# Kernel tuning notes

Measured on AMD Instinct MI355X. Metric: run time of the kernel, lower is better.

## Reference

```python
import jax, jax.numpy as jnp
import numpy as np
from jax import lax

B, D, H, W = 16, 256, 64, 64
P = 8  # patchsize
EPS = 1e-5


def setup_inputs() -> dict:
    key = jax.random.key(0)
    ks = jax.random.split(key, 8)
    s = 0.02
    return {
        "x": jax.random.normal(ks[0], (B, D, H, W), jnp.float32),
        "wq": jax.random.normal(ks[1], (D, D), jnp.float32) * s,
        "bq": jnp.zeros((D,), jnp.float32),
        "wk": jax.random.normal(ks[2], (D, D), jnp.float32) * s,
        "bk": jnp.zeros((D,), jnp.float32),
        "wv": jax.random.normal(ks[3], (D, D), jnp.float32) * s,
        "bv": jnp.zeros((D,), jnp.float32),
        "w_out": jax.random.normal(ks[4], (D, D, 3, 3), jnp.float32) * s,
        "b_out": jnp.zeros((D,), jnp.float32),
        "gamma": jnp.ones((D,), jnp.float32),
        "beta": jnp.zeros((D,), jnp.float32),
        "bn_mean": jnp.zeros((D,), jnp.float32),
        "bn_var": jnp.ones((D,), jnp.float32),
    }


def _conv1x1(x, w, b):
    # x: [b,c,h,w], w: [o,c] (1x1 conv) -> [b,o,h,w]
    return jnp.einsum('bchw,oc->bohw', x, w) + b[None, :, None, None]


def _to_patches(t, p):
    # [b,d,h,w] -> [b, p*p, d*hh*ww]  (matches view+permute(0,2,4,1,3,5)+view)
    b, d, h, w = t.shape
    hh, ww = h // p, w // p
    t = t.reshape(b, d, p, hh, p, ww).transpose(0, 2, 4, 1, 3, 5)
    return t.reshape(b, p * p, d * hh * ww)


def reference(x, wq, bq, wk, bk, wv, bv, w_out, b_out, gamma, beta, bn_mean, bn_var):
    b, d, h, w = x.shape
    p = P
    hh, ww = h // p, w // p

    q = _to_patches(_conv1x1(x, wq, bq), p)  # [b, p^2, d*hh*ww]
    k = _to_patches(_conv1x1(x, wk, bk), p)
    v = _to_patches(_conv1x1(x, wv, bv), p)

    scale = 1.0 / jnp.sqrt(jnp.asarray(q.shape[-1], q.dtype))
    scores = jnp.einsum('bqe,bke->bqk', q, k) * scale  # [b, p^2, p^2]
    attn = jax.nn.softmax(scores, axis=-1)
    out = jnp.einsum('bqk,bke->bqe', attn, v)  # [b, p^2, d*hh*ww]

    # [b,p,p,d,hh,ww] -> permute(0,3,1,4,2,5) -> [b,d,h,w]
    out = out.reshape(b, p, p, d, hh, ww).transpose(0, 3, 1, 4, 2, 5).reshape(b, d, h, w)

    # 3x3 conv, padding 1
    y = lax.conv_general_dilated(out, w_out, window_strides=(1, 1),
                                 padding=((1, 1), (1, 1)),
                                 dimension_numbers=('NCHW', 'OIHW', 'NCHW'))
    y = y + b_out[None, :, None, None]

    # BatchNorm2d (eval mode with running stats)
    inv = gamma / jnp.sqrt(bn_var + EPS)
    y = (y - bn_mean[None, :, None, None]) * inv[None, :, None, None] + beta[None, :, None, None]

    # LeakyReLU(0.2)
    return jnp.where(y >= 0, y, 0.2 * y)
```

## Files before the change

kernel.cpp:

```cpp
#include <hip/hip_runtime.h>
#include <hip/hip_bf16.h>

#define BB 16
#define SS 4096

typedef __attribute__((ext_vector_type(8))) short short8;
typedef __attribute__((ext_vector_type(4))) float float4v;

__global__ __launch_bounds__(256) void wprep_all(
    const float* __restrict__ wo, const float* __restrict__ wq,
    const float* __restrict__ wk, const float* __restrict__ wv,
    __hip_bfloat16* __restrict__ blob, __hip_bfloat16* __restrict__ blob_a) {
  const int bid = blockIdx.x;
  const int tid = threadIdx.x;
  if (bid < 288) {
    int chunk = bid * 256 + tid;
    int l = chunk & 63;
    int ob = (chunk >> 6) & 15;
    int cb = (chunk >> 10) & 7;
    int tap = chunk >> 13;
    int o = ob * 16 + (l & 15);
    int c0 = cb * 32 + (l >> 4) * 8;
    union { uint4 u; __hip_bfloat16 h[8]; } t;
#pragma unroll
    for (int j = 0; j < 8; ++j)
      t.h[j] = __float2bfloat16(wo[((size_t)(o * 256 + c0 + j)) * 9 + tap]);
    *reinterpret_cast<uint4*>(blob + (size_t)chunk * 8) = t.u;
  } else {
    int chunk = (bid - 288) * 256 + tid;
    int lane = chunk & 63;
    int ob = (chunk >> 6) & 15;
    int cb = (chunk >> 10) & 7;
    int which = chunk >> 13;
    const float* W = (which == 0) ? wq : (which == 1) ? wk : wv;
    int o = ob * 16 + (lane & 15);
    int c0 = cb * 32 + (lane >> 4) * 8;
    const float* p = W + o * 256 + c0;
    union { uint4 u; __hip_bfloat16 h[8]; } t;
#pragma unroll
    for (int j = 0; j < 8; ++j) t.h[j] = __float2bfloat16(p[j]);
    *reinterpret_cast<uint4*>(blob_a + (size_t)chunk * 8) = t.u;
  }
}

__global__ __launch_bounds__(256, 4) void qkv_mfma(
    const float* __restrict__ x, const __hip_bfloat16* __restrict__ blob,
    const float* __restrict__ bq, const float* __restrict__ bk,
    const float* __restrict__ bv,
    __hip_bfloat16* __restrict__ qb, __hip_bfloat16* __restrict__ kb,
    __hip_bfloat16* __restrict__ vb) {
  __shared__ short ls[2][64 * 40];
  const int which = blockIdx.z;
  const int b = blockIdx.y;
  const int s0 = blockIdx.x * 64;
  const float* bias = (which == 0) ? bq : (which == 1) ? bk : bv;
  __hip_bfloat16* outb = (which == 0) ? qb : kb;
  const int tid = threadIdx.x;
  const int wave = tid >> 6, lane = tid & 63;
  const int q = lane >> 4, m = lane & 15;
  const int sl = tid & 63;
  const int cg = tid >> 6;
  float4v acc[4][4] = {};

  const float* xbase = x + ((size_t)(b * 256 + cg * 8)) * SS + s0 + sl;
  float xr[8];
#pragma unroll
  for (int i = 0; i < 8; ++i) xr[i] = xbase[(size_t)i * SS];
  {
    union { uint4 u; __hip_bfloat16 h[8]; } t;
#pragma unroll
    for (int i = 0; i < 8; ++i) t.h[i] = __float2bfloat16(xr[i]);
    *reinterpret_cast<uint4*>(&ls[0][sl * 40 + cg * 8]) = t.u;
  }
  __syncthreads();

  for (int cb = 0; cb < 8; ++cb) {
    const short* cur = ls[cb & 1];
    short* nxt = ls[(cb + 1) & 1];
    if (cb < 7) {
#pragma unroll
      for (int i = 0; i < 8; ++i)
        xr[i] = xbase[(size_t)(cb + 1) * 32 * SS + (size_t)i * SS];
    }
    short8 af[4];
#pragma unroll
    for (int of = 0; of < 4; ++of)
      af[of] = *reinterpret_cast<const short8*>(
          blob +
          ((size_t)(((which * 8 + cb) * 16 + wave * 4 + of) * 64 + lane)) * 8);
    short8 xf[4];
#pragma unroll
    for (int sf = 0; sf < 4; ++sf)
      xf[sf] =
          *reinterpret_cast<const short8*>(&cur[(sf * 16 + m) * 40 + q * 8]);
#pragma unroll
    for (int of = 0; of < 4; ++of)
#pragma unroll
      for (int sf = 0; sf < 4; ++sf)
        acc[of][sf] = __builtin_amdgcn_mfma_f32_16x16x32_bf16(
            af[of], xf[sf], acc[of][sf], 0, 0, 0);
    if (cb < 7) {
      union { uint4 u; __hip_bfloat16 h[8]; } t;
#pragma unroll
      for (int i = 0; i < 8; ++i) t.h[i] = __float2bfloat16(xr[i]);
      *reinterpret_cast<uint4*>(&nxt[sl * 40 + cg * 8]) = t.u;
    }
    __syncthreads();
  }
  if (which == 2) {
    const int h = s0 >> 6;
#pragma unroll
    for (int of = 0; of < 4; ++of) {
      int o_base = wave * 64 + of * 16 + q * 4;
#pragma unroll
      for (int sf = 0; sf < 4; ++sf) {
        int w = sf * 16 + m;
        union { uint2 u; __hip_bfloat16 hh[4]; } t;
#pragma unroll
        for (int r = 0; r < 4; ++r)
          t.hh[r] = __float2bfloat16(acc[of][sf][r] + bias[o_base + r]);
        *reinterpret_cast<uint2*>(
            vb + ((size_t)((b * 64 + h) * 64 + w)) * 256 + o_base) = t.u;
      }
    }
  } else {
#pragma unroll
    for (int of = 0; of < 4; ++of) {
      int o_base = wave * 64 + of * 16 + q * 4;
#pragma unroll
      for (int r = 0; r < 4; ++r) {
        int o = o_base + r;
        float bi = bias[o];
        __hip_bfloat16* op = outb + ((size_t)(b * 256 + o)) * SS + s0 + m;
#pragma unroll
        for (int sf = 0; sf < 4; ++sf)
          op[sf * 16] = __float2bfloat16(acc[of][sf][r] + bi);
      }
    }
  }
}

__global__ __launch_bounds__(256) void scores_mfma(
    const __hip_bfloat16* __restrict__ qb, const __hip_bfloat16* __restrict__ kb,
    float* __restrict__ part) {
  const int b = blockIdx.y;
  const int d0 = blockIdx.x * 8;
  const int tid = threadIdx.x;
  const int wave = tid >> 6, lane = tid & 63;
  const int q = lane >> 4, m = lane & 15;
  const int t = wave * 16 + m;
  const int arow = (t >> 3) * 8;
  const int acol = (t & 7) * 8;
  float4v acc[4] = {};

  for (int dd = 0; dd < 8; ++dd) {
    const int d = d0 + dd;
    const __hip_bfloat16* qp = qb + ((size_t)(b * 256 + d)) * SS;
    const __hip_bfloat16* kp = kb + ((size_t)(b * 256 + d)) * SS;
#pragma unroll
    for (int khalf = 0; khalf < 2; ++khalf) {
      const int oh = khalf * 4 + q;
      short8 af = *reinterpret_cast<const short8*>(
          qp + (arow + oh) * 64 + acol);
      short8 bf[4];
#pragma unroll
      for (int nt = 0; nt < 4; ++nt) {
        int tp = nt * 16 + m;
        bf[nt] = *reinterpret_cast<const short8*>(
            kp + ((tp >> 3) * 8 + oh) * 64 + (tp & 7) * 8);
      }
#pragma unroll
      for (int nt = 0; nt < 4; ++nt)
        acc[nt] = __builtin_amdgcn_mfma_f32_16x16x32_bf16(af, bf[nt], acc[nt],
                                                          0, 0, 0);
    }
  }
  float* pp = part + ((size_t)(blockIdx.x * BB + b)) * 4096;
#pragma unroll
  for (int nt = 0; nt < 4; ++nt)
#pragma unroll
    for (int r = 0; r < 4; ++r)
      pp[(wave * 16 + q * 4 + r) * 64 + nt * 16 + m] = acc[nt][r];
}

__global__ __launch_bounds__(64) void softmax_kernel(
    const float* __restrict__ part, __hip_bfloat16* __restrict__ attnb) {
  const int t = blockIdx.x;
  const int b = blockIdx.y;
  const int lane = threadIdx.x;
  float v = 0.f;
#pragma unroll
  for (int sl = 0; sl < 32; ++sl)
    v += part[((size_t)(sl * BB + b)) * 4096 + t * 64 + lane];
  v *= 0.0078125f;
  float m = v;
#pragma unroll
  for (int off = 32; off >= 1; off >>= 1) m = fmaxf(m, __shfl_xor(m, off));
  float e = __expf(v - m);
  float s = e;
#pragma unroll
  for (int off = 32; off >= 1; off >>= 1) s += __shfl_xor(s, off);
  attnb[(b * 64 + t) * 64 + lane] = __float2bfloat16(e / s);
}

__global__ __launch_bounds__(256) void apply_mfma(
    const __hip_bfloat16* __restrict__ attnb, const __hip_bfloat16* __restrict__ vb,
    __hip_bfloat16* __restrict__ zb) {
  __shared__ short Vs[64][268];
  const int off = blockIdx.x;
  const int b = blockIdx.y;
  const int oh = off >> 3, ow = off & 7;
  const int tid = threadIdx.x;
#pragma unroll
  for (int i = 0; i < 8; ++i) {
    int chunk = i * 256 + tid;
    int tp = chunk >> 5;
    int cg = chunk & 31;
    int hh = (tp >> 3) * 8 + oh;
    int wwp = (tp & 7) * 8 + ow;
    uint4 val = *reinterpret_cast<const uint4*>(
        vb + ((size_t)((b * 64 + hh) * 64 + wwp)) * 256 + cg * 8);
    *reinterpret_cast<uint4*>(&Vs[tp][cg * 8]) = val;
  }
  __syncthreads();
  const int wave = tid >> 6, lane = tid & 63;
  const int q = lane >> 4, m = lane & 15;
  float4v acc[4][4] = {};
#pragma unroll
  for (int ks = 0; ks < 2; ++ks) {
    short8 af[4];
#pragma unroll
    for (int mt = 0; mt < 4; ++mt)
      af[mt] = *reinterpret_cast<const short8*>(
          attnb + (b * 64 + mt * 16 + m) * 64 + ks * 32 + q * 8);
    short8 bf[4];
#pragma unroll
    for (int nt = 0; nt < 4; ++nt) {
      int d = wave * 64 + nt * 16 + m;
      union { short8 v; short s[8]; } t;
#pragma unroll
      for (int j = 0; j < 8; ++j) t.s[j] = Vs[ks * 32 + q * 8 + j][d];
      bf[nt] = t.v;
    }
#pragma unroll
    for (int mt = 0; mt < 4; ++mt)
#pragma unroll
      for (int nt = 0; nt < 4; ++nt)
        acc[mt][nt] = __builtin_amdgcn_mfma_f32_16x16x32_bf16(
            af[mt], bf[nt], acc[mt][nt], 0, 0, 0);
  }
#pragma unroll
  for (int mt = 0; mt < 4; ++mt)
#pragma unroll
    for (int r = 0; r < 4; ++r) {
      int t = mt * 16 + q * 4 + r;
      int h = (t >> 3) * 8 + oh;
      int w = (t & 7) * 8 + ow;
      __hip_bfloat16* base = zb + ((size_t)((b * 64 + h) * 64 + w)) * 256;
#pragma unroll
      for (int nt = 0; nt < 4; ++nt)
        base[wave * 64 + nt * 16 + m] = __float2bfloat16(acc[mt][nt][r]);
    }
}

__global__ __launch_bounds__(256) void conv_mfma(
    const __hip_bfloat16* __restrict__ z, const __hip_bfloat16* __restrict__ blob,
    const float* __restrict__ bo, const float* __restrict__ gm,
    const float* __restrict__ bt, const float* __restrict__ mn,
    const float* __restrict__ vr, float* __restrict__ out) {
  __shared__ short zs[2][3 * 66 * 40];
  const int idx0 = blockIdx.x;
  const int h = (idx0 & 7) * 8 + ((idx0 >> 3) & 7);
  const int b = idx0 >> 6;
  const int tid = threadIdx.x;
  const int wave = tid >> 6, lane = tid & 63;
  const int q = lane >> 4, m = lane & 15;
  float4v acc[4][4] = {};

  int s_r[4], s_wp[4], s_cg[4];
  bool s_ok[4], s_act[4];
  const __hip_bfloat16* s_base[4];
#pragma unroll
  for (int k = 0; k < 4; ++k) {
    int idx = tid + k * 256;
    bool act = idx < 792;
    int cg = idx & 3;
    int t2 = idx >> 2;
    int wpos = act ? (t2 % 66) : 0;
    int r = act ? (t2 / 66) : 0;
    int h_in = h - 1 + r;
    int w_in = wpos - 1;
    bool ok = act && h_in >= 0 && h_in < 64 && w_in >= 0 && w_in < 64;
    if (!act) { r = 0; wpos = 0; cg = 0; }
    s_r[k] = r; s_wp[k] = wpos; s_cg[k] = cg;
    s_ok[k] = ok; s_act[k] = act;
    s_base[k] = z + ((size_t)((b * 64 + h_in) * 64 + w_in)) * 256 + cg * 8;
  }

  uint4 pf[4];
#pragma unroll
  for (int k = 0; k < 4; ++k)
    pf[k] = s_ok[k] ? *reinterpret_cast<const uint4*>(s_base[k])
                    : make_uint4(0u, 0u, 0u, 0u);
#pragma unroll
  for (int k = 0; k < 4; ++k)
    if (s_act[k])
      *reinterpret_cast<uint4*>(
          &zs[0][(s_r[k] * 66 + s_wp[k]) * 40 + s_cg[k] * 8]) = pf[k];

  short8 wfb[2][4];
#pragma unroll
  for (int of = 0; of < 4; ++of)
    wfb[0][of] = *reinterpret_cast<const short8*>(
        blob + ((size_t)((0 * 16 + wave * 4 + of) * 64 + lane)) * 8);
  __syncthreads();

#pragma unroll 2
  for (int cb = 0; cb < 8; ++cb) {
    const short* cur = zs[cb & 1];
    short* nxt = zs[(cb + 1) & 1];
    if (cb < 7) {
#pragma unroll
      for (int k = 0; k < 4; ++k)
        pf[k] = s_ok[k] ? *reinterpret_cast<const uint4*>(
                              s_base[k] + (size_t)(cb + 1) * 32)
                        : make_uint4(0u, 0u, 0u, 0u);
    }
#pragma unroll
    for (int tap = 0; tap < 9; ++tap) {
      const int kh = tap / 3, kw = tap % 3;
      const int p = (cb + tap) & 1;
      {
        const int ntap = (tap == 8) ? 0 : tap + 1;
        const int ncb = (tap == 8) ? cb + 1 : cb;
        if (ncb < 8) {
#pragma unroll
          for (int of = 0; of < 4; ++of)
            wfb[p ^ 1][of] = *reinterpret_cast<const short8*>(
                blob +
                ((size_t)(((ntap * 8 + ncb) * 16 + wave * 4 + of) * 64 + lane)) *
                    8);
        }
      }
      short8 zf[4];
#pragma unroll
      for (int wfi = 0; wfi < 4; ++wfi) {
        int wpos = wfi * 16 + m + kw;
        zf[wfi] = *reinterpret_cast<const short8*>(
            &cur[(kh * 66 + wpos) * 40 + q * 8]);
      }
#pragma unroll
      for (int of = 0; of < 4; ++of)
#pragma unroll
        for (int wfi = 0; wfi < 4; ++wfi)
          acc[of][wfi] = __builtin_amdgcn_mfma_f32_16x16x32_bf16(
              wfb[p][of], zf[wfi], acc[of][wfi], 0, 0, 0);
    }
    if (cb < 7) {
#pragma unroll
      for (int k = 0; k < 4; ++k)
        if (s_act[k])
          *reinterpret_cast<uint4*>(
              &nxt[(s_r[k] * 66 + s_wp[k]) * 40 + s_cg[k] * 8]) = pf[k];
    }
    __syncthreads();
  }
#pragma unroll
  for (int of = 0; of < 4; ++of) {
    int o_base = wave * 64 + of * 16 + q * 4;
#pragma unroll
    for (int r = 0; r < 4; ++r) {
      int o = o_base + r;
      float sc = gm[o] * rsqrtf(vr[o] + 1e-5f);
      float sh = bt[o] + (bo[o] - mn[o]) * sc;
#pragma unroll
      for (int wfi = 0; wfi < 4; ++wfi) {
        float y = acc[of][wfi][r] * sc + sh;
        y = (y >= 0.f) ? y : 0.2f * y;
        out[(((size_t)(b * 256 + o)) * 64 + h) * 64 + wfi * 16 + m] = y;
      }
    }
  }
}

extern "C" void kernel_launch(void* const* d_in, const int* in_sizes, int n_in,
                              void* d_out, int out_size, void* d_ws,
                              size_t ws_size, hipStream_t stream) {
  (void)in_sizes; (void)n_in; (void)out_size; (void)ws_size;
  const float* x  = (const float*)d_in[0];
  const float* wq = (const float*)d_in[1];
  const float* bq = (const float*)d_in[2];
  const float* wk = (const float*)d_in[3];
  const float* bk = (const float*)d_in[4];
  const float* wv = (const float*)d_in[5];
  const float* bv = (const float*)d_in[6];
  const float* wo = (const float*)d_in[7];
  const float* bo = (const float*)d_in[8];
  const float* gm = (const float*)d_in[9];
  const float* bt = (const float*)d_in[10];
  const float* mn = (const float*)d_in[11];
  const float* vr = (const float*)d_in[12];
  float* out = (float*)d_out;

  char* ws = (char*)d_ws;
  __hip_bfloat16* qb = (__hip_bfloat16*)(ws);
  __hip_bfloat16* kb = (__hip_bfloat16*)(ws + 33554432);
  __hip_bfloat16* attnb = (__hip_bfloat16*)(ws + 67371008);
  __hip_bfloat16* blob = (__hip_bfloat16*)(ws + 67502080);
  __hip_bfloat16* vb = (__hip_bfloat16*)d_out;
  __hip_bfloat16* blob_a = (__hip_bfloat16*)((char*)d_out + 33554432);
  float* part = (float*)((char*)d_out + 37748736);

  wprep_all<<<384, 256, 0, stream>>>(wo, wq, wk, wv, blob, blob_a);
  qkv_mfma<<<dim3(64, BB, 3), 256, 0, stream>>>(x, blob_a, bq, bk, bv,
                                                qb, kb, vb);
  scores_mfma<<<dim3(32, BB), 256, 0, stream>>>(qb, kb, part);
  softmax_kernel<<<dim3(64, BB), 64, 0, stream>>>(part, attnb);
  apply_mfma<<<dim3(64, BB), 256, 0, stream>>>(attnb, vb, qb );
  conv_mfma<<<dim3(BB * 64), 256, 0, stream>>>(qb, blob, bo, gm, bt, mn, vr,
                                               out);
}
```

Measured before the change: 316.8 us.

## Split V projection and store V in patch-transposed layout for apply

Splits the QKV projection into a Q/K kernel and a separate V kernel. The V kernel writes V in a per-patch-offset, channel-major layout, so apply_mfma can load MFMA B fragments straight from global memory and no longer stages V through LDS with strided gathers. The Q/K kernel swaps the MFMA operand order so each lane holds contiguous spatial outputs and can store 4 bf16 values at once. The trade-off is that the V kernel now does scattered 2-byte stores and there is one extra kernel launch.

```diff
diff --git a/kernel.cpp b/kernel.cpp
--- a/kernel.cpp
+++ b/kernel.cpp
@@ -43,17 +43,15 @@
   }
 }
 
-__global__ __launch_bounds__(256, 4) void qkv_mfma(
+__global__ __launch_bounds__(256, 4) void qk_mfma(
     const float* __restrict__ x, const __hip_bfloat16* __restrict__ blob,
     const float* __restrict__ bq, const float* __restrict__ bk,
-    const float* __restrict__ bv,
-    __hip_bfloat16* __restrict__ qb, __hip_bfloat16* __restrict__ kb,
-    __hip_bfloat16* __restrict__ vb) {
+    __hip_bfloat16* __restrict__ qb, __hip_bfloat16* __restrict__ kb) {
   __shared__ short ls[2][64 * 40];
   const int which = blockIdx.z;
   const int b = blockIdx.y;
   const int s0 = blockIdx.x * 64;
-  const float* bias = (which == 0) ? bq : (which == 1) ? bk : bv;
+  const float* bias = (which == 0) ? bq : bk;
   __hip_bfloat16* outb = (which == 0) ? qb : kb;
   const int tid = threadIdx.x;
   const int wave = tid >> 6, lane = tid & 63;
@@ -98,7 +96,7 @@
 #pragma unroll
       for (int sf = 0; sf < 4; ++sf)
         acc[of][sf] = __builtin_amdgcn_mfma_f32_16x16x32_bf16(
-            af[of], xf[sf], acc[of][sf], 0, 0, 0);
+            xf[sf], af[of], acc[of][sf], 0, 0, 0);
     if (cb < 7) {
       union { uint4 u; __hip_bfloat16 h[8]; } t;
 #pragma unroll
@@ -107,34 +105,95 @@
     }
     __syncthreads();
   }
-  if (which == 2) {
-    const int h = s0 >> 6;
-#pragma unroll
-    for (int of = 0; of < 4; ++of) {
-      int o_base = wave * 64 + of * 16 + q * 4;
+#pragma unroll
+  for (int of = 0; of < 4; ++of) {
+    int o = wave * 64 + of * 16 + m;
+    float bi = bias[o];
+    __hip_bfloat16* op = outb + (size_t)(b * 256 + o) * SS + s0;
+#pragma unroll
+    for (int sf = 0; sf < 4; ++sf) {
+      union { uint2 u; __hip_bfloat16 hh[4]; } t;
+#pragma unroll
+      for (int r = 0; r < 4; ++r)
+        t.hh[r] = __float2bfloat16(acc[of][sf][r] + bi);
+      *reinterpret_cast<uint2*>(op + sf * 16 + q * 4) = t.u;
+    }
+  }
+}
+
+__global__ __launch_bounds__(256, 4) void v_mfma(
+    const float* __restrict__ x, const __hip_bfloat16* __restrict__ blob,
+    const float* __restrict__ bv, __hip_bfloat16* __restrict__ vt) {
+  __shared__ short ls[2][64 * 40];
+  const int b = blockIdx.y;
+  const int s0 = blockIdx.x * 64;
+  const int h = blockIdx.x;
+  const int pi = h >> 3, hhi = h & 7;
+  const int tid = threadIdx.x;
+  const int wave = tid >> 6, lane = tid & 63;
+  const int q = lane >> 4, m = lane & 15;
+  const int sl = tid & 63;
+  const int cg = tid >> 6;
+  float4v acc[4][4] = {};
+
+  const float* xbase = x + ((size_t)(b * 256 + cg * 8)) * SS + s0 + sl;
+  float xr[8];
+#pragma unroll
+  for (int i = 0; i < 8; ++i) xr[i] = xbase[(size_t)i * SS];
+  {
+    union { uint4 u; __hip_bfloat16 h8[8]; } t;
+#pragma unroll
+    for (int i = 0; i < 8; ++i) t.h8[i] = __float2bfloat16(xr[i]);
+    *reinterpret_cast<uint4*>(&ls[0][sl * 40 + cg * 8]) = t.u;
+  }
+  __syncthreads();
+
+  for (int cb = 0; cb < 8; ++cb) {
+    const short* cur = ls[cb & 1];
+    short* nxt = ls[(cb + 1) & 1];
+    if (cb < 7) {
+#pragma unroll
+      for (int i = 0; i < 8; ++i)
+        xr[i] = xbase[(size_t)(cb + 1) * 32 * SS + (size_t)i * SS];
+    }
+    short8 af[4];
+#pragma unroll
+    for (int of = 0; of < 4; ++of)
+      af[of] = *reinterpret_cast<const short8*>(
+          blob +
+          ((size_t)(((2 * 8 + cb) * 16 + wave * 4 + of) * 64 + lane)) * 8);
+    short8 xf[4];
+#pragma unroll
+    for (int sf = 0; sf < 4; ++sf)
+      xf[sf] =
+          *reinterpret_cast<const short8*>(&cur[(sf * 16 + m) * 40 + q * 8]);
+#pragma unroll
+    for (int of = 0; of < 4; ++of)
+#pragma unroll
+      for (int sf = 0; sf < 4; ++sf)
+        acc[of][sf] = __builtin_amdgcn_mfma_f32_16x16x32_bf16(
+            af[of], xf[sf], acc[of][sf], 0, 0, 0);
+    if (cb < 7) {
+      union { uint4 u; __hip_bfloat16 h8[8]; } t;
+#pragma unroll
+      for (int i = 0; i < 8; ++i) t.h8[i] = __float2bfloat16(xr[i]);
+      *reinterpret_cast<uint4*>(&nxt[sl * 40 + cg * 8]) = t.u;
+    }
+    __syncthreads();
+  }
+  __hip_bfloat16* vb0 = vt + ((size_t)(b * 8 + hhi)) * 8 * 256 * 64;
+#pragma unroll
+  for (int of = 0; of < 4; ++of) {
+    int o_base = wave * 64 + of * 16 + q * 4;
+#pragma unroll
+    for (int r = 0; r < 4; ++r) {
+      int o = o_base + r;
+      float bi = bv[o];
 #pragma unroll
       for (int sf = 0; sf < 4; ++sf) {
         int w = sf * 16 + m;
-        union { uint2 u; __hip_bfloat16 hh[4]; } t;
-#pragma unroll
-        for (int r = 0; r < 4; ++r)
-          t.hh[r] = __float2bfloat16(acc[of][sf][r] + bias[o_base + r]);
-        *reinterpret_cast<uint2*>(
-            vb + ((size_t)((b * 64 + h) * 64 + w)) * 256 + o_base) = t.u;
-      }
-    }
-  } else {
-#pragma unroll
-    for (int of = 0; of < 4; ++of) {
-      int o_base = wave * 64 + of * 16 + q * 4;
-#pragma unroll
-      for (int r = 0; r < 4; ++r) {
-        int o = o_base + r;
-        float bi = bias[o];
-        __hip_bfloat16* op = outb + ((size_t)(b * 256 + o)) * SS + s0 + m;
-#pragma unroll
-        for (int sf = 0; sf < 4; ++sf)
-          op[sf * 16] = __float2bfloat16(acc[of][sf][r] + bi);
+        vb0[((size_t)((w & 7) * 256 + o)) * 64 + pi * 8 + (w >> 3)] =
+            __float2bfloat16(acc[of][sf][r] + bi);
       }
     }
   }
@@ -204,27 +263,16 @@
 }
 
 __global__ __launch_bounds__(256) void apply_mfma(
-    const __hip_bfloat16* __restrict__ attnb, const __hip_bfloat16* __restrict__ vb,
+    const __hip_bfloat16* __restrict__ attnb, const __hip_bfloat16* __restrict__ vt,
     __hip_bfloat16* __restrict__ zb) {
-  __shared__ short Vs[64][268];
   const int off = blockIdx.x;
   const int b = blockIdx.y;
   const int oh = off >> 3, ow = off & 7;
   const int tid = threadIdx.x;
-#pragma unroll
-  for (int i = 0; i < 8; ++i) {
-    int chunk = i * 256 + tid;
-    int tp = chunk >> 5;
-    int cg = chunk & 31;
-    int hh = (tp >> 3) * 8 + oh;
-    int wwp = (tp & 7) * 8 + ow;
-    uint4 val = *reinterpret_cast<const uint4*>(
-        vb + ((size_t)((b * 64 + hh) * 64 + wwp)) * 256 + cg * 8);
-    *reinterpret_cast<uint4*>(&Vs[tp][cg * 8]) = val;
-  }
-  __syncthreads();
   const int wave = tid >> 6, lane = tid & 63;
   const int q = lane >> 4, m = lane & 15;
+  const __hip_bfloat16* vbase =
+      vt + ((size_t)((b * 8 + oh) * 8 + ow)) * 256 * 64;
   float4v acc[4][4] = {};
 #pragma unroll
   for (int ks = 0; ks < 2; ++ks) {
@@ -237,10 +285,8 @@
 #pragma unroll
     for (int nt = 0; nt < 4; ++nt) {
       int d = wave * 64 + nt * 16 + m;
-      union { short8 v; short s[8]; } t;
-#pragma unroll
-      for (int j = 0; j < 8; ++j) t.s[j] = Vs[ks * 32 + q * 8 + j][d];
-      bf[nt] = t.v;
+      bf[nt] = *reinterpret_cast<const short8*>(
+          vbase + (size_t)d * 64 + ks * 32 + q * 8);
     }
 #pragma unroll
     for (int mt = 0; mt < 4; ++mt)
@@ -407,16 +453,16 @@
   __hip_bfloat16* kb = (__hip_bfloat16*)(ws + 33554432);
   __hip_bfloat16* attnb = (__hip_bfloat16*)(ws + 67371008);
   __hip_bfloat16* blob = (__hip_bfloat16*)(ws + 67502080);
-  __hip_bfloat16* vb = (__hip_bfloat16*)d_out;
+  __hip_bfloat16* vt = (__hip_bfloat16*)d_out;
   __hip_bfloat16* blob_a = (__hip_bfloat16*)((char*)d_out + 33554432);
   float* part = (float*)((char*)d_out + 37748736);
 
   wprep_all<<<384, 256, 0, stream>>>(wo, wq, wk, wv, blob, blob_a);
-  qkv_mfma<<<dim3(64, BB, 3), 256, 0, stream>>>(x, blob_a, bq, bk, bv,
-                                                qb, kb, vb);
+  qk_mfma<<<dim3(64, BB, 2), 256, 0, stream>>>(x, blob_a, bq, bk, qb, kb);
+  v_mfma<<<dim3(64, BB), 256, 0, stream>>>(x, blob_a, bv, vt);
   scores_mfma<<<dim3(32, BB), 256, 0, stream>>>(qb, kb, part);
   softmax_kernel<<<dim3(64, BB), 64, 0, stream>>>(part, attnb);
-  apply_mfma<<<dim3(64, BB), 256, 0, stream>>>(attnb, vb, qb );
+  apply_mfma<<<dim3(64, BB), 256, 0, stream>>>(attnb, vt, qb );
   conv_mfma<<<dim3(BB * 64), 256, 0, stream>>>(qb, blob, bo, gm, bt, mn, vr,
                                                out);
 }
```

Result: slower. 361.5 us (+14.1%).
